# Kernel optimization log

Measured on AMD Instinct MI355X. Metric: run time of the kernel, lower is better.

Reference implementation:

```python
import jax, jax.numpy as jnp
import numpy as np

INPUT_DIM = 1024
NUM_TARGETS = 128
BATCH = 32768


def setup_inputs() -> dict:
    key = jax.random.key(0)
    kx, kw, kb = jax.random.split(key, 3)
    x = jax.random.normal(kx, (BATCH, INPUT_DIM), dtype=jnp.float32)
    # Fused view of num_targets independent nn.Linear(input_dim, 1) layers:
    # column t of W / entry t of b are the weights/bias of layer t.
    bound = 1.0 / np.sqrt(INPUT_DIM)  # torch Linear default init range
    W = jax.random.uniform(kw, (INPUT_DIM, NUM_TARGETS), minval=-bound, maxval=bound, dtype=jnp.float32)
    b = jax.random.uniform(kb, (NUM_TARGETS,), minval=-bound, maxval=bound, dtype=jnp.float32)
    return {"x": x, "W": W, "b": b}


def reference(x, W, b):
    # Equivalent to concatenating sigmoid(Linear_t(x)) over t along last dim:
    # one fused matmul [B,D]x[D,T] + bias + sigmoid.
    return jax.nn.sigmoid(x @ W + b)
```

## Files before the change

### kernel.cpp

```cpp
#include <hip/hip_runtime.h>
#include <hip/hip_bf16.h>


typedef __bf16 bf16x8 __attribute__((ext_vector_type(8)));
typedef float  f32x4  __attribute__((ext_vector_type(4)));

#define DIM   1024
#define NT    128
#define BATCH 32768

__global__ __launch_bounds__(256) void prep_w(const float* __restrict__ W,
                                              __bf16* __restrict__ wsW) {
    int idx = blockIdx.x * 256 + threadIdx.x;
    int j = idx & 7;
    int l = (idx >> 3) & 63;
    int c = (idx >> 9) & 7;
    int s = idx >> 12;
    int k = s * 32 + (l >> 4) * 8 + j;
    int n = c * 16 + (l & 15);
    wsW[idx] = (__bf16)W[k * NT + n];
}

__device__ __forceinline__ bf16x8 cvt_bf16x8(float4 a0, float4 a1) {
    bf16x8 af;
    af[0] = (__bf16)a0.x; af[1] = (__bf16)a0.y;
    af[2] = (__bf16)a0.z; af[3] = (__bf16)a0.w;
    af[4] = (__bf16)a1.x; af[5] = (__bf16)a1.y;
    af[6] = (__bf16)a1.z; af[7] = (__bf16)a1.w;
    return af;
}

__global__ __launch_bounds__(256) void gemm_bias_sigmoid(
        const float* __restrict__ x,
        const __hip_bfloat16* __restrict__ wsWh,
        const float* __restrict__ bias,
        float* __restrict__ out) {
    const bf16x8* __restrict__ wsW8 = (const bf16x8*)wsWh;
    __shared__ bf16x8 ldsW[4096];

    const int tid  = threadIdx.x;
    const int lane = tid & 63;
    const int wave = tid >> 6;
    const int q    = lane >> 4;
    const int r    = lane & 15;
    const int row0 = blockIdx.x * 64 + wave * 16;

    const float* xA = x + (size_t)(row0 + r) * DIM + q * 8;

    f32x4 acc[8];
#pragma unroll
    for (int c = 0; c < 8; ++c)
        acc[c] = (f32x4){0.f, 0.f, 0.f, 0.f};

    float4 S0[8], S1[8];

#pragma unroll
    for (int i = 0; i < 4; ++i) {
        const float* ap = xA + (size_t)i * 32;
        S0[2 * i]     = *(const float4*)ap;
        S0[2 * i + 1] = *(const float4*)(ap + 4);
    }

    for (int p = 0; p < 4; ++p) {
        __syncthreads();
#pragma unroll
        for (int i = 0; i < 16; ++i) {
            const int e = tid + i * 256;
            ldsW[e] = wsW8[p * 4096 + e];
        }
#pragma unroll
        for (int i = 0; i < 4; ++i) {
            const float* ap = xA + (size_t)(p * 8 + 4 + i) * 32;
            S1[2 * i]     = *(const float4*)ap;
            S1[2 * i + 1] = *(const float4*)(ap + 4);
        }
        __syncthreads();

#pragma unroll
        for (int sl = 0; sl < 4; ++sl) {
            const bf16x8 af = cvt_bf16x8(S0[2 * sl], S0[2 * sl + 1]);
#pragma unroll
            for (int c = 0; c < 8; ++c) {
                const bf16x8 bf = ldsW[(sl * 8 + c) * 64 + lane];
                acc[c] = __builtin_amdgcn_mfma_f32_16x16x32_bf16(af, bf, acc[c], 0, 0, 0);
            }
        }
        if (p < 3) {
#pragma unroll
            for (int i = 0; i < 4; ++i) {
                const float* ap = xA + (size_t)((p + 1) * 8 + i) * 32;
                S0[2 * i]     = *(const float4*)ap;
                S0[2 * i + 1] = *(const float4*)(ap + 4);
            }
        }
#pragma unroll
        for (int sl = 4; sl < 8; ++sl) {
            const bf16x8 af = cvt_bf16x8(S1[2 * (sl - 4)], S1[2 * (sl - 4) + 1]);
#pragma unroll
            for (int c = 0; c < 8; ++c) {
                const bf16x8 bf = ldsW[(sl * 8 + c) * 64 + lane];
                acc[c] = __builtin_amdgcn_mfma_f32_16x16x32_bf16(af, bf, acc[c], 0, 0, 0);
            }
        }
    }

#pragma unroll
    for (int c = 0; c < 8; ++c) {
        const float bv = bias[c * 16 + r];
#pragma unroll
        for (int reg = 0; reg < 4; ++reg) {
            const int row = row0 + q * 4 + reg;
            float v = acc[c][reg] + bv;
            v = 1.0f / (1.0f + __expf(-v));
            out[(size_t)row * NT + c * 16 + r] = v;
        }
    }
}

extern "C" void kernel_launch(void* const* d_in, const int* in_sizes, int n_in,
                              void* d_out, int out_size, void* d_ws, size_t ws_size,
                              hipStream_t stream) {
    const float* x = (const float*)d_in[0];
    const float* W = (const float*)d_in[1];
    const float* b = (const float*)d_in[2];
    float* out     = (float*)d_out;
    __bf16* wsW    = (__bf16*)d_ws;

    prep_w<<<DIM * NT / 256, 256, 0, stream>>>(W, wsW);
    gemm_bias_sigmoid<<<BATCH / 64, 256, 0, stream>>>(
        x, (const __hip_bfloat16*)wsW, b, out);
}
```

Measured before the change: 202.3 us.

## Double-buffer W staging via direct global-to-LDS loads with manual waitcnt pipeline

The W tile is now staged in two smaller LDS buffers of 128 K-rows each. The loads use global_load_lds, which moves data straight to LDS without passing through registers, and each wave stages its own slice. A hand-written s_waitcnt/barrier schedule overlaps fetching the next W and x chunks with MFMA compute on the current chunk. LDS use drops from 64KB to 64KB split into two buffers, and launch bounds now request 2 blocks per CU. The aim is to hide global latency and cut register pressure from the W copy. In exchange it relies on fragile manual vmcnt counting, where a wrong count could cause races.

Result: no change. 202.6 us (+0.1%).

```diff
diff --git a/kernel.cpp b/kernel.cpp
--- a/kernel.cpp
+++ b/kernel.cpp
@@ -8,6 +8,12 @@
 #define DIM   1024
 #define NT    128
 #define BATCH 32768
+
+#define WAITVM16()  asm volatile("s_waitcnt vmcnt(16)" ::: "memory")
+#define WAITVM0()   asm volatile("s_waitcnt vmcnt(0)"  ::: "memory")
+#define WAITLGKM0() asm volatile("s_waitcnt lgkmcnt(0)" ::: "memory")
+#define CFENCE()    asm volatile("" ::: "memory")
+#define BAR()       __builtin_amdgcn_s_barrier()
 
 __global__ __launch_bounds__(256) void prep_w(const float* __restrict__ W,
                                               __bf16* __restrict__ wsW) {
@@ -30,13 +36,44 @@
     return af;
 }
 
-__global__ __launch_bounds__(256) void gemm_bias_sigmoid(
+__device__ __forceinline__ void stage8(const bf16x8* g, bf16x8* l) {
+#pragma unroll
+    for (int i = 0; i < 8; ++i)
+        __builtin_amdgcn_global_load_lds(
+            (const __attribute__((address_space(1))) void*)(g + i * 64),
+            (__attribute__((address_space(3))) void*)(l + i * 64),
+            16, 0, 0);
+}
+
+__device__ __forceinline__ void loada8(float4* S, const float* xA, int P) {
+#pragma unroll
+    for (int sl = 0; sl < 4; ++sl) {
+        const float* ap = xA + (size_t)(P * 4 + sl) * 32;
+        S[2 * sl]     = *(const float4*)ap;
+        S[2 * sl + 1] = *(const float4*)(ap + 4);
+    }
+}
+
+__device__ __forceinline__ void compute8(const float4* S, const bf16x8* bb,
+                                         int lane, f32x4* acc) {
+#pragma unroll
+    for (int sl = 0; sl < 4; ++sl) {
+        const bf16x8 af = cvt_bf16x8(S[2 * sl], S[2 * sl + 1]);
+#pragma unroll
+        for (int c = 0; c < 8; ++c) {
+            const bf16x8 bf = bb[(sl * 8 + c) * 64 + lane];
+            acc[c] = __builtin_amdgcn_mfma_f32_16x16x32_bf16(af, bf, acc[c], 0, 0, 0);
+        }
+    }
+}
+
+__global__ __launch_bounds__(256, 2) void gemm_bias_sigmoid(
         const float* __restrict__ x,
         const __hip_bfloat16* __restrict__ wsWh,
         const float* __restrict__ bias,
         float* __restrict__ out) {
     const bf16x8* __restrict__ wsW8 = (const bf16x8*)wsWh;
-    __shared__ bf16x8 ldsW[4096];
+    __shared__ bf16x8 ldsW[2][2048];
 
     const int tid  = threadIdx.x;
     const int lane = tid & 63;
@@ -46,63 +83,45 @@
     const int row0 = blockIdx.x * 64 + wave * 16;
 
     const float* xA = x + (size_t)(row0 + r) * DIM + q * 8;
+    const bf16x8* gW = wsW8 + wave * 512 + lane;
+    bf16x8* lW0 = &ldsW[0][wave * 512];
+    bf16x8* lW1 = &ldsW[1][wave * 512];
 
     f32x4 acc[8];
 #pragma unroll
     for (int c = 0; c < 8; ++c)
         acc[c] = (f32x4){0.f, 0.f, 0.f, 0.f};
 
-    float4 S0[8], S1[8];
+    float4 SA[8], SB[8];
 
-#pragma unroll
-    for (int i = 0; i < 4; ++i) {
-        const float* ap = xA + (size_t)i * 32;
-        S0[2 * i]     = *(const float4*)ap;
-        S0[2 * i + 1] = *(const float4*)(ap + 4);
-    }
+    stage8(gW, lW0);
+    loada8(SA, xA, 0);
+    stage8(gW + 2048, lW1);
+    loada8(SB, xA, 1);
+    WAITVM16();
+    BAR(); CFENCE();
 
-    for (int p = 0; p < 4; ++p) {
-        __syncthreads();
-#pragma unroll
-        for (int i = 0; i < 16; ++i) {
-            const int e = tid + i * 256;
-            ldsW[e] = wsW8[p * 4096 + e];
-        }
-#pragma unroll
-        for (int i = 0; i < 4; ++i) {
-            const float* ap = xA + (size_t)(p * 8 + 4 + i) * 32;
-            S1[2 * i]     = *(const float4*)ap;
-            S1[2 * i + 1] = *(const float4*)(ap + 4);
-        }
-        __syncthreads();
+#define STEP(P, S, LWB, BB)                                        \
+    compute8(S, BB, lane, acc);                                    \
+    WAITLGKM0();                                                   \
+    BAR(); CFENCE();                \
+    stage8(gW + (size_t)(P + 2) * 2048, LWB);      \
+    loada8(S, xA, P + 2);                          \
+    WAITVM16();                          \
+    BAR(); CFENCE();
 
-#pragma unroll
-        for (int sl = 0; sl < 4; ++sl) {
-            const bf16x8 af = cvt_bf16x8(S0[2 * sl], S0[2 * sl + 1]);
-#pragma unroll
-            for (int c = 0; c < 8; ++c) {
-                const bf16x8 bf = ldsW[(sl * 8 + c) * 64 + lane];
-                acc[c] = __builtin_amdgcn_mfma_f32_16x16x32_bf16(af, bf, acc[c], 0, 0, 0);
-            }
-        }
-        if (p < 3) {
-#pragma unroll
-            for (int i = 0; i < 4; ++i) {
-                const float* ap = xA + (size_t)((p + 1) * 8 + i) * 32;
-                S0[2 * i]     = *(const float4*)ap;
-                S0[2 * i + 1] = *(const float4*)(ap + 4);
-            }
-        }
-#pragma unroll
-        for (int sl = 4; sl < 8; ++sl) {
-            const bf16x8 af = cvt_bf16x8(S1[2 * (sl - 4)], S1[2 * (sl - 4) + 1]);
-#pragma unroll
-            for (int c = 0; c < 8; ++c) {
-                const bf16x8 bf = ldsW[(sl * 8 + c) * 64 + lane];
-                acc[c] = __builtin_amdgcn_mfma_f32_16x16x32_bf16(af, bf, acc[c], 0, 0, 0);
-            }
-        }
-    }
+    STEP(0, SA, lW0, &ldsW[0][0])
+    STEP(1, SB, lW1, &ldsW[1][0])
+    STEP(2, SA, lW0, &ldsW[0][0])
+    STEP(3, SB, lW1, &ldsW[1][0])
+    STEP(4, SA, lW0, &ldsW[0][0])
+    STEP(5, SB, lW1, &ldsW[1][0])
+#undef STEP
+
+    compute8(SA, &ldsW[0][0], lane, acc);
+    WAITVM0();
+    BAR(); CFENCE();
+    compute8(SB, &ldsW[1][0], lane, acc);
 
 #pragma unroll
     for (int c = 0; c < 8; ++c) {
```

## Read packed bf16 weights directly from global memory instead of staging in LDS

Applied to the files above, without the earlier changes.

Removes the 64KB LDS staging of the pre-packed bf16 weight tile and the barriers around it. Each wave now loads its B fragments straight from global memory, relying on L1/L2 to serve the 256KB weight buffer that all blocks share, and the explicit double-buffering of x loads is dropped in favour of a fully unrolled loop. Launch bounds request two blocks per CU, which the lower LDS use makes possible. The trade is that weight traffic goes through the cache hierarchy on every use, and the hand-written prefetch of x is gone.

Result: slower. 248.8 us (+23.0%).

```diff
diff --git a/kernel.cpp b/kernel.cpp
--- a/kernel.cpp
+++ b/kernel.cpp
@@ -30,13 +30,12 @@
     return af;
 }
 
-__global__ __launch_bounds__(256) void gemm_bias_sigmoid(
+__global__ __launch_bounds__(256, 2) void gemm_bias_sigmoid(
         const float* __restrict__ x,
         const __hip_bfloat16* __restrict__ wsWh,
         const float* __restrict__ bias,
         float* __restrict__ out) {
     const bf16x8* __restrict__ wsW8 = (const bf16x8*)wsWh;
-    __shared__ bf16x8 ldsW[4096];
 
     const int tid  = threadIdx.x;
     const int lane = tid & 63;
@@ -45,62 +44,24 @@
     const int r    = lane & 15;
     const int row0 = blockIdx.x * 64 + wave * 16;
 
-    const float* xA = x + (size_t)(row0 + r) * DIM + q * 8;
+    const float*  xA  = x + (size_t)(row0 + r) * DIM + q * 8;
+    const bf16x8* gB  = wsW8 + lane;
 
     f32x4 acc[8];
 #pragma unroll
     for (int c = 0; c < 8; ++c)
         acc[c] = (f32x4){0.f, 0.f, 0.f, 0.f};
 
-    float4 S0[8], S1[8];
-
 #pragma unroll
-    for (int i = 0; i < 4; ++i) {
-        const float* ap = xA + (size_t)i * 32;
-        S0[2 * i]     = *(const float4*)ap;
-        S0[2 * i + 1] = *(const float4*)(ap + 4);
-    }
-
-    for (int p = 0; p < 4; ++p) {
-        __syncthreads();
+    for (int s = 0; s < 32; ++s) {
+        const float* ap = xA + (size_t)s * 32;
+        const float4 a0 = *(const float4*)ap;
+        const float4 a1 = *(const float4*)(ap + 4);
+        const bf16x8 af = cvt_bf16x8(a0, a1);
 #pragma unroll
-        for (int i = 0; i < 16; ++i) {
-            const int e = tid + i * 256;
-            ldsW[e] = wsW8[p * 4096 + e];
-        }
-#pragma unroll
-        for (int i = 0; i < 4; ++i) {
-            const float* ap = xA + (size_t)(p * 8 + 4 + i) * 32;
-            S1[2 * i]     = *(const float4*)ap;
-            S1[2 * i + 1] = *(const float4*)(ap + 4);
-        }
-        __syncthreads();
-
-#pragma unroll
-        for (int sl = 0; sl < 4; ++sl) {
-            const bf16x8 af = cvt_bf16x8(S0[2 * sl], S0[2 * sl + 1]);
-#pragma unroll
-            for (int c = 0; c < 8; ++c) {
-                const bf16x8 bf = ldsW[(sl * 8 + c) * 64 + lane];
-                acc[c] = __builtin_amdgcn_mfma_f32_16x16x32_bf16(af, bf, acc[c], 0, 0, 0);
-            }
-        }
-        if (p < 3) {
-#pragma unroll
-            for (int i = 0; i < 4; ++i) {
-                const float* ap = xA + (size_t)((p + 1) * 8 + i) * 32;
-                S0[2 * i]     = *(const float4*)ap;
-                S0[2 * i + 1] = *(const float4*)(ap + 4);
-            }
-        }
-#pragma unroll
-        for (int sl = 4; sl < 8; ++sl) {
-            const bf16x8 af = cvt_bf16x8(S1[2 * (sl - 4)], S1[2 * (sl - 4) + 1]);
-#pragma unroll
-            for (int c = 0; c < 8; ++c) {
-                const bf16x8 bf = ldsW[(sl * 8 + c) * 64 + lane];
-                acc[c] = __builtin_amdgcn_mfma_f32_16x16x32_bf16(af, bf, acc[c], 0, 0, 0);
-            }
+        for (int c = 0; c < 8; ++c) {
+            const bf16x8 bf = gB[(s * 8 + c) * 64];
+            acc[c] = __builtin_amdgcn_mfma_f32_16x16x32_bf16(af, bf, acc[c], 0, 0, 0);
         }
     }
 
```
